# Kernel optimization log

Measured on AMD Instinct MI355X. Metric: run time of the kernel, lower is better.

## Reference

```python
import jax, jax.numpy as jnp
import numpy as np


def _rope(x, token_positions, theta):
    # x: [B, H, S, D], token_positions: [S]
    d = x.shape[-1]
    freqs = 1.0 / theta ** (jnp.arange(0, d, 2, dtype=jnp.float32) / d)  # [D/2]
    angles = token_positions.astype(jnp.float32)[:, None] * freqs[None, :]  # [S, D/2]
    cos, sin = jnp.cos(angles), jnp.sin(angles)
    x_even = x[..., 0::2]
    x_odd = x[..., 1::2]
    new_even = x_even * cos - x_odd * sin
    new_odd = x_even * sin + x_odd * cos
    return jnp.stack([new_even, new_odd], axis=-1).reshape(x.shape)


def setup_inputs() -> dict:
    key = jax.random.key(0)
    ks = jax.random.split(key, 5)
    B, S, D = 2, 2048, 1024
    scale = 1.0 / np.sqrt(D)
    return {
        "x": jax.random.normal(ks[0], (B, S, D), dtype=jnp.float32),
        "Wq": jax.random.normal(ks[1], (D, D), dtype=jnp.float32) * scale,
        "Wk": jax.random.normal(ks[2], (D, D), dtype=jnp.float32) * scale,
        "Wv": jax.random.normal(ks[3], (D, D), dtype=jnp.float32) * scale,
        "Wo": jax.random.normal(ks[4], (D, D), dtype=jnp.float32) * scale,
        "token_positions": jnp.arange(S, dtype=jnp.int32),
        "rope_theta": 10000,
    }


def reference(x, Wq, Wk, Wv, Wo, token_positions, rope_theta):
    B, S, Dm = x.shape
    H = 16
    d_k = Dm // H
    # nn.Linear(bias=False): y = x @ W.T
    def proj(W):
        y = jnp.einsum('bsd,ed->bse', x, W)
        return y.reshape(B, S, H, d_k).transpose(0, 2, 1, 3)  # [B,H,S,Dk]
    q = _rope(proj(Wq), token_positions, float(rope_theta))
    k = _rope(proj(Wk), token_positions, float(rope_theta))
    v = proj(Wv)
    scores = jnp.einsum('bhqd,bhkd->bhqk', q, k) / jnp.sqrt(jnp.float32(d_k))
    causal = jnp.tril(jnp.ones((S, S), dtype=bool))
    scores = jnp.where(causal, scores, -jnp.inf)
    p = jax.nn.softmax(scores, axis=-1)
    vals = jnp.einsum('bhqk,bhkd->bhqd', p, v)
    out = vals.transpose(0, 2, 1, 3).reshape(B, S, Dm)
    return jnp.einsum('bsd,ed->bse', out, Wo)
```

## Files before the change

kernel.cpp:

```cpp
#include <hip/hip_runtime.h>
#include <hip/hip_bf16.h>
#include <stdint.h>

typedef __attribute__((ext_vector_type(8))) __bf16 bf16x8;
typedef __attribute__((ext_vector_type(4))) float f32x4;
typedef __hip_bfloat16 bf16;

#define GLDS(g, l) __builtin_amdgcn_global_load_lds( \
    (const __attribute__((address_space(1))) void*)(g), \
    (__attribute__((address_space(3))) void*)(l), 16, 0, 0)

#define SCALE_Q 0.18033688f
#define MFIX 12.0f

#define OFF_XB     ((size_t)0)
#define OFF_WQKVB  ((size_t)8388608)
#define OFF_WOB    ((size_t)14680064)
#define OFF_QB     ((size_t)16777216)
#define OFF_KB     ((size_t)25165824)
#define OFF_VTB    ((size_t)33554432)
#define OFF_CS     ((size_t)41943040)
#define OFF_SN     ((size_t)42205184)

__global__ void prep_kernel(const float* __restrict__ x, const float* __restrict__ wq,
                            const float* __restrict__ wk, const float* __restrict__ wv,
                            const float* __restrict__ wo,
                            bf16* __restrict__ xb, bf16* __restrict__ wqkvb,
                            bf16* __restrict__ wob,
                            const int* __restrict__ pos, const void* __restrict__ theta_p,
                            float* __restrict__ cst, float* __restrict__ snt)
{
    const int region = blockIdx.y;
    if (region == 5) {
        if (blockIdx.x >= 256) return;
        const int t = blockIdx.x * 256 + threadIdx.x;
        const int s = t >> 5, i = t & 31;
        const int ti = ((const int*)theta_p)[0];
        const float theta = (ti > 0 && ti < 100000000) ? (float)ti : ((const float*)theta_p)[0];
        const float fr = expf(-(float)i * (1.0f / 32.0f) * logf(theta));
        const float ang = (float)pos[s] * fr;
        cst[t] = cosf(ang);
        snt[t] = sinf(ang);
        return;
    }
    const float* src;
    bf16* dst;
    int count;
    switch (region) {
        case 0:  src = x;  dst = xb;              count = 4096 * 1024; break;
        case 1:  src = wq; dst = wqkvb;           count = 1024 * 1024; break;
        case 2:  src = wk; dst = wqkvb + 1048576; count = 1024 * 1024; break;
        case 3:  src = wv; dst = wqkvb + 2097152; count = 1024 * 1024; break;
        default: src = wo; dst = wob;             count = 1024 * 1024; break;
    }
    const int i = (blockIdx.x * 256 + threadIdx.x) * 4;
    if (i >= count) return;
    const float4 v = *(const float4*)(src + i);
    union { bf16 h[4]; short4 s4; } u;
    u.h[0] = __float2bfloat16(v.x);
    u.h[1] = __float2bfloat16(v.y);
    u.h[2] = __float2bfloat16(v.z);
    u.h[3] = __float2bfloat16(v.w);
    *(short4*)(dst + i) = u.s4;
}

template<int MODE, int BM>
__global__ __launch_bounds__(256) void gemm_bt(
    const bf16* __restrict__ A, const bf16* __restrict__ B,
    const int K, const int N,
    float* __restrict__ outf,
    bf16* __restrict__ qb, bf16* __restrict__ kb, bf16* __restrict__ vtb,
    const float* __restrict__ cst, const float* __restrict__ snt)
{
    constexpr int NF = BM / 32;
    __shared__ __align__(16) bf16 Asl[BM * 64];
    __shared__ __align__(16) bf16 Bsl[128 * 64];
    const int tid = threadIdx.x;
    const int wave = tid >> 6, lane = tid & 63;
    const int lr = lane & 15, lk = lane >> 4;

    const int nwg = gridDim.x * gridDim.y;
    const int flat = blockIdx.y * gridDim.x + blockIdx.x;
    const int wg = (flat & 7) * (nwg >> 3) + (flat >> 3);
    const int m0 = (wg % gridDim.x) * BM;
    const int n0 = (wg / gridDim.x) * 128;

    const int wm = (wave >> 1) * (BM / 2);
    const int wn = (wave & 1) * 64;
    const int srow = tid >> 3, sseg = tid & 7;
    const int swel = (sseg ^ (srow & 7)) * 8;

    f32x4 acc[NF][4] = {};

    const bf16* aRow = A + (size_t)(m0 + srow) * K + swel;
    const bf16* bRow = B + (size_t)(n0 + srow) * K + swel;
    char* lA = (char*)Asl + tid * 16;
    char* lB = (char*)Bsl + tid * 16;
    const size_t rowK32 = (size_t)32 * K;

    for (int k0 = 0; k0 < K; k0 += 64) {
#pragma unroll
        for (int g = 0; g < NF; ++g)
            GLDS(aRow + k0 + g * rowK32, lA + g * 4096);
#pragma unroll
        for (int g = 0; g < 4; ++g)
            GLDS(bRow + k0 + g * rowK32, lB + g * 4096);
        __syncthreads();
#pragma unroll
        for (int kk = 0; kk < 2; ++kk) {
            const int s = kk * 4 + lk;
            bf16x8 af[NF], bfr[4];
#pragma unroll
            for (int i = 0; i < NF; ++i) {
                const int R = wm + i * 16 + lr;
                af[i] = *(const bf16x8*)((const char*)Asl + R * 128 + (((s) ^ (R & 7)) << 4));
            }
#pragma unroll
            for (int j = 0; j < 4; ++j) {
                const int R = wn + j * 16 + lr;
                bfr[j] = *(const bf16x8*)((const char*)Bsl + R * 128 + (((s) ^ (R & 7)) << 4));
            }
#pragma unroll
            for (int i = 0; i < NF; ++i)
#pragma unroll
                for (int j = 0; j < 4; ++j)
                    acc[i][j] = __builtin_amdgcn_mfma_f32_16x16x32_bf16(af[i], bfr[j], acc[i][j], 0, 0, 0);
        }
        __syncthreads();
    }

    if constexpr (MODE == 1) {
#pragma unroll
        for (int i = 0; i < NF; ++i)
#pragma unroll
            for (int j = 0; j < 4; ++j)
#pragma unroll
                for (int r = 0; r < 4; ++r) {
                    const int row = m0 + wm + i * 16 + lk * 4 + r;
                    const int col = n0 + wn + j * 16 + lr;
                    outf[(size_t)row * N + col] = acc[i][j][r];
                }
    } else {
        const int matn = n0 >> 10;
#pragma unroll
        for (int i = 0; i < NF; ++i)
#pragma unroll
            for (int j = 0; j < 4; ++j)
#pragma unroll
                for (int r = 0; r < 4; ++r) {
                    const int row = m0 + wm + i * 16 + lk * 4 + r;
                    const int col = n0 + wn + j * 16 + lr;
                    float v = acc[i][j][r];
                    float p = __shfl_xor(v, 1);
                    const int e = col & 1023;
                    const int h = e >> 6;
                    const int dd = e & 63;
                    const int b = row >> 11;
                    const int s = row & 2047;
                    const size_t bhi = (size_t)(b * 16 + h);
                    if (matn == 2) {
                        vtb[(bhi * 64 + dd) * 2048 + s] = __float2bfloat16(v);
                    } else {
                        const float cs = cst[s * 32 + (dd >> 1)];
                        const float sn = snt[s * 32 + (dd >> 1)];
                        const float rv = (dd & 1) ? (p * sn + v * cs) : (v * cs - p * sn);
                        if (matn == 0)
                            qb[(bhi * 2048 + s) * 64 + dd] = __float2bfloat16(rv * SCALE_Q);
                        else
                            kb[(bhi * 2048 + s) * 64 + dd] = __float2bfloat16(rv);
                    }
                }
    }
}

__global__ __launch_bounds__(256) void attn_kernel(
    const bf16* __restrict__ qb, const bf16* __restrict__ kb,
    const bf16* __restrict__ vtb, bf16* __restrict__ attnb)
{
    __shared__ __align__(16) bf16 Kl[2][64 * 64];
    __shared__ __align__(16) bf16 Vl[2][64 * 64];
    __shared__ __align__(16) bf16 Pl[4][2][16][72];
    const int tid = threadIdx.x;
    const int wave = tid >> 6, lane = tid & 63;
    const int lr = lane & 15, lk = lane >> 4;
    const int tA = blockIdx.x;
    const int tB = 31 - tA;
    const int bh = blockIdx.y;
    const int qA = tA * 64 + wave * 16;
    const int qB = tB * 64 + wave * 16;

    const bf16* Qp = qb + (size_t)bh * 2048 * 64;
    const bf16* Kp = kb + (size_t)bh * 2048 * 64;
    const bf16* Vp = vtb + (size_t)bh * 64 * 2048;

    const int srow = tid >> 3;
    const int sseg = tid & 7;
    const int sw16 = (sseg ^ (srow & 7)) * 16;
    const char* kg = (const char*)Kp + (size_t)srow * 128 + sw16;
    const char* vg = (const char*)Vp + (size_t)srow * 4096 + sw16;

#define STAGE(kt_, c_) do {                                              \
        const char* kgt = kg + (size_t)(kt_) * 8192;                     \
        GLDS(kgt,              &Kl[c_][0] + tid * 8);                    \
        GLDS(kgt + 32 * 128,   &Kl[c_][0] + 2048 + tid * 8);             \
        const char* vgt = vg + (size_t)(kt_) * 128;                      \
        GLDS(vgt,              &Vl[c_][0] + tid * 8);                    \
        GLDS(vgt + 32 * 4096,  &Vl[c_][0] + 2048 + tid * 8);             \
    } while (0)

    bf16x8 qfA[2], qfB[2];
#pragma unroll
    for (int ks = 0; ks < 2; ++ks) {
        qfA[ks] = *(const bf16x8*)(Qp + (qA + lr) * 64 + ks * 32 + lk * 8);
        qfB[ks] = *(const bf16x8*)(Qp + (qB + lr) * 64 + ks * 32 + lk * 8);
    }

    float sA = 0.f, sB = 0.f;
    f32x4 oA[4] = {}, oB[4] = {};

    STAGE(0, 0);

    const int xoff = (lr & 7) * 8;

    for (int kt = 0; kt <= tB; ++kt) {
        const int c = kt & 1;
        const int kv0 = kt * 64;
        const bool doA = (kt <= tA);
        if (kt < tB) {
            STAGE(kt + 1, c ^ 1);
            asm volatile("s_waitcnt vmcnt(4)" ::: "memory");
        } else {
            asm volatile("s_waitcnt vmcnt(0)" ::: "memory");
        }
        __builtin_amdgcn_s_barrier();
        __builtin_amdgcn_sched_barrier(0);
        const bf16* Kc = &Kl[c][0];
        const bf16* Vc = &Vl[c][0];

        f32x4 scB[4] = {}, scA[4] = {};
#pragma unroll
        for (int ks = 0; ks < 2; ++ks) {
            bf16x8 kf[4];
#pragma unroll
            for (int j = 0; j < 4; ++j)
                kf[j] = *(const bf16x8*)(Kc + (j * 16 + lr) * 64 + ((ks * 32 + lk * 8) ^ xoff));
            __builtin_amdgcn_s_setprio(1);
#pragma unroll
            for (int j = 0; j < 4; ++j)
                scB[j] = __builtin_amdgcn_mfma_f32_16x16x32_bf16(kf[j], qfB[ks], scB[j], 0, 0, 0);
            if (doA) {
#pragma unroll
                for (int j = 0; j < 4; ++j)
                    scA[j] = __builtin_amdgcn_mfma_f32_16x16x32_bf16(kf[j], qfA[ks], scA[j], 0, 0, 0);
            }
            __builtin_amdgcn_s_setprio(0);
        }

        bf16x8 vf[2][4];
#pragma unroll
        for (int ks = 0; ks < 2; ++ks)
#pragma unroll
            for (int j = 0; j < 4; ++j)
                vf[ks][j] = *(const bf16x8*)(Vc + (j * 16 + lr) * 64 + ((ks * 32 + lk * 8) ^ xoff));

        auto smx = [&](f32x4* sc, float& ssum, int qX, bool diag, int st) {
            if (diag) {
#pragma unroll
                for (int j = 0; j < 4; ++j)
#pragma unroll
                    for (int r = 0; r < 4; ++r)
                        if (kv0 + j * 16 + lk * 4 + r > qX + lr) sc[j][r] = -1e30f;
            }
            float l0 = 0.f, l1 = 0.f, l2 = 0.f, l3 = 0.f;
#pragma unroll
            for (int j = 0; j < 4; ++j) {
                float pv[4];
                pv[0] = exp2f(sc[j][0] - MFIX);
                pv[1] = exp2f(sc[j][1] - MFIX);
                pv[2] = exp2f(sc[j][2] - MFIX);
                pv[3] = exp2f(sc[j][3] - MFIX);
                l0 += pv[0]; l1 += pv[1]; l2 += pv[2]; l3 += pv[3];
                union { bf16 h[4]; ushort4 s4; } u;
#pragma unroll
                for (int r = 0; r < 4; ++r) u.h[r] = __float2bfloat16(pv[r]);
                *(ushort4*)(&Pl[wave][st][lr][j * 16 + lk * 4]) = u.s4;
            }
            ssum += (l0 + l1) + (l2 + l3);
        };
        auto pv = [&](f32x4* o, int st) {
#pragma unroll
            for (int ks = 0; ks < 2; ++ks) {
                const bf16x8 pf = *(const bf16x8*)(&Pl[wave][st][lr][ks * 32 + lk * 8]);
                __builtin_amdgcn_s_setprio(1);
#pragma unroll
                for (int j = 0; j < 4; ++j)
                    o[j] = __builtin_amdgcn_mfma_f32_16x16x32_bf16(vf[ks][j], pf, o[j], 0, 0, 0);
                __builtin_amdgcn_s_setprio(0);
            }
        };

        smx(scB, sB, qB, kt == tB, 1);
        if (doA) smx(scA, sA, qA, kt == tA, 0);
        pv(oB, 1);
        if (doA) pv(oA, 0);

        __builtin_amdgcn_sched_barrier(0);
        __builtin_amdgcn_s_barrier();
    }

    const int b = bh >> 4, h = bh & 15;
    auto epi = [&](float ssum, f32x4* o, int qX) {
        float s = ssum;
        s += __shfl_xor(s, 16);
        s += __shfl_xor(s, 32);
        const float inv = 1.0f / s;
        const int qq = qX + lr;
        bf16* dst = attnb + (size_t)(b * 2048 + qq) * 1024 + h * 64 + lk * 4;
#pragma unroll
        for (int j = 0; j < 4; ++j) {
            union { bf16 h4[4]; ushort4 s4; } u;
#pragma unroll
            for (int r = 0; r < 4; ++r) u.h4[r] = __float2bfloat16(o[j][r] * inv);
            *(ushort4*)(dst + j * 16) = u.s4;
        }
    };
    epi(sA, oA, qA);
    epi(sB, oB, qB);
#undef STAGE
}

extern "C" void kernel_launch(void* const* d_in, const int* in_sizes, int n_in,
                              void* d_out, int out_size, void* d_ws, size_t ws_size,
                              hipStream_t stream)
{
    const float* x   = (const float*)d_in[0];
    const float* wq  = (const float*)d_in[1];
    const float* wk  = (const float*)d_in[2];
    const float* wv  = (const float*)d_in[3];
    const float* wo  = (const float*)d_in[4];
    const int*   pos = (const int*)d_in[5];
    const void* theta = d_in[6];

    char* ws = (char*)d_ws;
    bf16* xb    = (bf16*)(ws + OFF_XB);
    bf16* attnb = (bf16*)(ws + OFF_XB);
    bf16* wqkvb = (bf16*)(ws + OFF_WQKVB);
    bf16* wob   = (bf16*)(ws + OFF_WOB);
    bf16* qb    = (bf16*)(ws + OFF_QB);
    bf16* kb    = (bf16*)(ws + OFF_KB);
    bf16* vtb   = (bf16*)(ws + OFF_VTB);
    float* cst  = (float*)(ws + OFF_CS);
    float* snt  = (float*)(ws + OFF_SN);

    prep_kernel<<<dim3(4096, 6), 256, 0, stream>>>(x, wq, wk, wv, wo, xb, wqkvb, wob,
                                                   pos, theta, cst, snt);
    gemm_bt<0, 128><<<dim3(32, 24), 256, 0, stream>>>(xb, wqkvb, 1024, 3072, nullptr,
                                                      qb, kb, vtb, cst, snt);
    attn_kernel<<<dim3(16, 32), 256, 0, stream>>>(qb, kb, vtb, attnb);
    gemm_bt<1, 64><<<dim3(64, 8), 256, 0, stream>>>(attnb, wob, 1024, 1024, (float*)d_out,
                                                    nullptr, nullptr, nullptr, nullptr, nullptr);
}
```

Measured before the change: 142.4 us.

## Split long causal attention strips across two blocks and add combine kernel

The attention grid grows from 16 to 24 blocks per head. For the longest query strips (the 8 longest tB values), the key loop is split in half. One block handles the first half alongside its paired short strip, and a new block handles the second half. Unnormalized partial outputs and row sums are written to scratch buffers, and a new combine kernel adds them and normalizes. This is meant to raise parallelism and shorten the critical path per CU, but it adds an extra launch, extra global traffic, and an intermediate bf16 rounding of unnormalized partials.

```diff
diff --git a/kernel.cpp b/kernel.cpp
--- a/kernel.cpp
+++ b/kernel.cpp
@@ -3,6 +3,7 @@
 #include <stdint.h>
 
 typedef __attribute__((ext_vector_type(8))) __bf16 bf16x8;
+typedef __attribute__((ext_vector_type(8))) unsigned short u16x8;
 typedef __attribute__((ext_vector_type(4))) float f32x4;
 typedef __hip_bfloat16 bf16;
 
@@ -15,12 +16,19 @@
 
 #define OFF_XB     ((size_t)0)
 #define OFF_WQKVB  ((size_t)8388608)
+#define OFF_PBUF   ((size_t)8388608)
+#define OFF_SB0    ((size_t)10485760)
+#define OFF_SB1    ((size_t)10551296)
 #define OFF_WOB    ((size_t)14680064)
 #define OFF_QB     ((size_t)16777216)
 #define OFF_KB     ((size_t)25165824)
 #define OFF_VTB    ((size_t)33554432)
 #define OFF_CS     ((size_t)41943040)
 #define OFF_SN     ((size_t)42205184)
+
+static __device__ __forceinline__ float b2f(unsigned short u) {
+    union { unsigned u32; float f; } c; c.u32 = (unsigned)u << 16; return c.f;
+}
 
 __global__ void prep_kernel(const float* __restrict__ x, const float* __restrict__ wq,
                             const float* __restrict__ wk, const float* __restrict__ wv,
@@ -175,7 +183,8 @@
 
 __global__ __launch_bounds__(256) void attn_kernel(
     const bf16* __restrict__ qb, const bf16* __restrict__ kb,
-    const bf16* __restrict__ vtb, bf16* __restrict__ attnb)
+    const bf16* __restrict__ vtb, bf16* __restrict__ attnb,
+    bf16* __restrict__ pbuf, float* __restrict__ sb0, float* __restrict__ sb1)
 {
     __shared__ __align__(16) bf16 Kl[2][64 * 64];
     __shared__ __align__(16) bf16 Vl[2][64 * 64];
@@ -183,10 +192,25 @@
     const int tid = threadIdx.x;
     const int wave = tid >> 6, lane = tid & 63;
     const int lr = lane & 15, lk = lane >> 4;
-    const int tA = blockIdx.x;
-    const int tB = 31 - tA;
+    const int xi = blockIdx.x;
     const int bh = blockIdx.y;
-    const int qA = tA * 64 + wave * 16;
+
+    int tA, tB, ktBeg, ktEnd;
+    bool hasA, partB, z1;
+    if (xi < 16) {
+        tA = xi; tB = 31 - xi;
+        const int hk = (tB + 2) >> 1;
+        z1 = false; hasA = true;
+        if (xi < 8) { partB = true;  ktBeg = 0; ktEnd = hk - 1; }
+        else        { partB = false; ktBeg = 0; ktEnd = tB; }
+    } else {
+        const int x = xi - 16;
+        tA = -1; tB = 31 - x;
+        const int hk = (tB + 2) >> 1;
+        z1 = true; hasA = false; partB = true;
+        ktBeg = hk; ktEnd = tB;
+    }
+    const int qA = (hasA ? tA : 0) * 64 + wave * 16;
     const int qB = tB * 64 + wave * 16;
 
     const bf16* Qp = qb + (size_t)bh * 2048 * 64;
@@ -218,15 +242,15 @@
     float sA = 0.f, sB = 0.f;
     f32x4 oA[4] = {}, oB[4] = {};
 
-    STAGE(0, 0);
+    STAGE(ktBeg, ktBeg & 1);
 
     const int xoff = (lr & 7) * 8;
 
-    for (int kt = 0; kt <= tB; ++kt) {
+    for (int kt = ktBeg; kt <= ktEnd; ++kt) {
         const int c = kt & 1;
         const int kv0 = kt * 64;
-        const bool doA = (kt <= tA);
-        if (kt < tB) {
+        const bool doA = hasA && (kt <= tA);
+        if (kt < ktEnd) {
             STAGE(kt + 1, c ^ 1);
             asm volatile("s_waitcnt vmcnt(4)" ::: "memory");
         } else {
@@ -309,13 +333,12 @@
     }
 
     const int b = bh >> 4, h = bh & 15;
-    auto epi = [&](float ssum, f32x4* o, int qX) {
+    auto epiF = [&](float ssum, f32x4* o, int qX) {
         float s = ssum;
         s += __shfl_xor(s, 16);
         s += __shfl_xor(s, 32);
         const float inv = 1.0f / s;
-        const int qq = qX + lr;
-        bf16* dst = attnb + (size_t)(b * 2048 + qq) * 1024 + h * 64 + lk * 4;
+        bf16* dst = attnb + (size_t)(b * 2048 + qX + lr) * 1024 + h * 64 + lk * 4;
 #pragma unroll
         for (int j = 0; j < 4; ++j) {
             union { bf16 h4[4]; ushort4 s4; } u;
@@ -324,9 +347,64 @@
             *(ushort4*)(dst + j * 16) = u.s4;
         }
     };
-    epi(sA, oA, qA);
-    epi(sB, oB, qB);
+    if (hasA) epiF(sA, oA, qA);
+    if (!partB) {
+        epiF(sB, oB, qB);
+    } else {
+        const int x = z1 ? (xi - 16) : xi;
+        const int strip = x * 32 + bh;
+        float s = sB;
+        s += __shfl_xor(s, 16);
+        s += __shfl_xor(s, 32);
+        bf16* dstO;
+        float* dstS;
+        if (!z1) {
+            dstO = attnb + (size_t)(b * 2048 + qB + lr) * 1024 + h * 64 + lk * 4;
+            dstS = sb0 + strip * 64 + wave * 16 + lr;
+        } else {
+            dstO = pbuf + ((size_t)strip * 64 + wave * 16 + lr) * 64 + lk * 4;
+            dstS = sb1 + strip * 64 + wave * 16 + lr;
+        }
+#pragma unroll
+        for (int j = 0; j < 4; ++j) {
+            union { bf16 h4[4]; ushort4 s4; } u;
+#pragma unroll
+            for (int r = 0; r < 4; ++r) u.h4[r] = __float2bfloat16(oB[j][r]);
+            *(ushort4*)(dstO + j * 16) = u.s4;
+        }
+        if (lk == 0) *dstS = s;
+    }
 #undef STAGE
+}
+
+__global__ void combine_kernel(const bf16* __restrict__ pbuf,
+                               const float* __restrict__ sb0, const float* __restrict__ sb1,
+                               bf16* __restrict__ attnb)
+{
+    const int strip = blockIdx.x;
+    const int x = strip >> 5, bh = strip & 31;
+    const int tB = 31 - x;
+    const int b = bh >> 4, h = bh & 15;
+    const int t = threadIdx.x;
+    const int row = t >> 2;
+    const int dseg = (t & 3) * 16;
+    const int qq = tB * 64 + row;
+    const float s = sb0[strip * 64 + row] + sb1[strip * 64 + row];
+    const float inv = 1.0f / s;
+    bf16* dst = attnb + (size_t)(b * 2048 + qq) * 1024 + h * 64 + dseg;
+    const bf16* p1 = pbuf + ((size_t)strip * 64 + row) * 64 + dseg;
+    u16x8 a0 = *(const u16x8*)(dst);
+    u16x8 a1 = *(const u16x8*)(dst + 8);
+    u16x8 c0 = *(const u16x8*)(p1);
+    u16x8 c1 = *(const u16x8*)(p1 + 8);
+    union { bf16 h8[8]; u16x8 v; } o0, o1;
+#pragma unroll
+    for (int i = 0; i < 8; ++i) {
+        o0.h8[i] = __float2bfloat16((b2f(a0[i]) + b2f(c0[i])) * inv);
+        o1.h8[i] = __float2bfloat16((b2f(a1[i]) + b2f(c1[i])) * inv);
+    }
+    *(u16x8*)(dst)     = o0.v;
+    *(u16x8*)(dst + 8) = o1.v;
 }
 
 extern "C" void kernel_launch(void* const* d_in, const int* in_sizes, int n_in,
@@ -345,6 +423,9 @@
     bf16* xb    = (bf16*)(ws + OFF_XB);
     bf16* attnb = (bf16*)(ws + OFF_XB);
     bf16* wqkvb = (bf16*)(ws + OFF_WQKVB);
+    bf16* pbuf  = (bf16*)(ws + OFF_PBUF);
+    float* sb0  = (float*)(ws + OFF_SB0);
+    float* sb1  = (float*)(ws + OFF_SB1);
     bf16* wob   = (bf16*)(ws + OFF_WOB);
     bf16* qb    = (bf16*)(ws + OFF_QB);
     bf16* kb    = (bf16*)(ws + OFF_KB);
@@ -356,7 +437,8 @@
                                                    pos, theta, cst, snt);
     gemm_bt<0, 128><<<dim3(32, 24), 256, 0, stream>>>(xb, wqkvb, 1024, 3072, nullptr,
                                                       qb, kb, vtb, cst, snt);
-    attn_kernel<<<dim3(16, 32), 256, 0, stream>>>(qb, kb, vtb, attnb);
+    attn_kernel<<<dim3(24, 32), 256, 0, stream>>>(qb, kb, vtb, attnb, pbuf, sb0, sb1);
+    combine_kernel<<<256, 256, 0, stream>>>(pbuf, sb0, sb1, attnb);
     gemm_bt<1, 64><<<dim3(64, 8), 256, 0, stream>>>(attnb, wob, 1024, 1024, (float*)d_out,
                                                     nullptr, nullptr, nullptr, nullptr, nullptr);
 }
```

Measured after the change: 160.6 us. 1.13x slower.
